# Kernel optimization log

Hardware: AMD Instinct MI355X
Metric: run time of the kernel (lower is better)

Reference implementation:

```python
import jax, jax.numpy as jnp
import numpy as np

NUM_LAYERS = 4
N_EDGE_TYPES = 3
RBAR = 1
DIM = 128
N_NODES = 50000
N_EDGES = 600000
N_HOP_LAYERS = NUM_LAYERS * (NUM_LAYERS + 1) // 2  # 10
EPS = 1e-12


def setup_inputs() -> dict:
    key = jax.random.key(0)
    ks = jax.random.split(key, 8)
    x = jax.random.normal(ks[0], (N_NODES, DIM), dtype=jnp.float32)
    edge_index = jax.random.randint(ks[1], (2, N_EDGES), 0, N_NODES, dtype=jnp.int64)
    edge_hop = jax.random.randint(ks[2], (N_EDGES,), 0, NUM_LAYERS + 1, dtype=jnp.int64)
    edge_type = jax.random.randint(ks[3], (N_EDGES,), 0, N_EDGE_TYPES, dtype=jnp.int64)
    scale = 1.0 / np.sqrt(DIM)
    W_edge = jax.random.normal(ks[4], (N_EDGE_TYPES, DIM, DIM), dtype=jnp.float32) * scale
    b_edge = jnp.zeros((N_EDGE_TYPES, DIM), dtype=jnp.float32)
    W_hop = jax.random.normal(ks[5], (N_HOP_LAYERS, DIM, DIM), dtype=jnp.float32) * scale
    b_hop = jnp.zeros((N_HOP_LAYERS, DIM), dtype=jnp.float32)
    return {"x": x, "edge_index": edge_index, "edge_hop": edge_hop,
            "edge_type": edge_type, "W_edge": W_edge, "b_edge": b_edge,
            "W_hop": W_hop, "b_hop": b_hop}


def _conv(h_in, W, b, src, dst, mask, n_nodes):
    """GraphConv sub-layer on a masked edge subset: sum_{j->i, mask} (x_j W) + b."""
    h = h_in @ W                                  # [N, d]
    msg = h[src] * mask[:, None]                  # [E, d], masked gather
    agg = jax.ops.segment_sum(msg, dst, num_segments=n_nodes)
    return agg + b


def reference(x, edge_index, edge_hop, edge_type, W_edge, b_edge, W_hop, b_hop):
    n_nodes = x.shape[0]
    src, dst = edge_index[0], edge_index[1]
    xs = []
    cur = x
    idx = 0  # sequential consumption of hop sub-layers (next(modules))
    for t in range(NUM_LAYERS):
        xs.append(cur)
        acc = jnp.zeros_like(cur)
        # relation-specific sub-layers, always on x[t]
        for e in range(N_EDGE_TYPES):
            mask = (edge_type == e).astype(cur.dtype)
            acc = acc + _conv(xs[t], W_edge[e], b_edge[e], src, dst, mask, n_nodes)
        # delay / k-hop sub-layers, k = 1..t+1, reading delayed state x[t-delay]
        for k in range(1, t + 2):
            delay = max(k - RBAR, 0)
            mask = (edge_hop == k).astype(cur.dtype)
            acc = acc + _conv(xs[t - delay], W_hop[idx], b_hop[idx], src, dst, mask, n_nodes)
            idx += 1
        cur = xs[t] + jax.nn.relu(acc)
        # F.normalize(p=2, dim=-1): x / max(||x||_2, eps)
        norm = jnp.linalg.norm(cur, axis=-1, keepdims=True)
        cur = cur / jnp.maximum(norm, EPS)
    return cur
```

## Files before the change

kernel.cpp:

```cpp
#include <hip/hip_runtime.h>
#include <hip/hip_bf16.h>

#define DIM 128
#define NLAYER 4

typedef _Float16 f16x8 __attribute__((ext_vector_type(8)));
typedef _Float16 f16x2 __attribute__((ext_vector_type(2)));
typedef float f32x4 __attribute__((ext_vector_type(4)));

static constexpr int PHYS[10] = {0, 4, 1, 0, 5, 2, 1, 4, 6, 3};


__global__ void k_count(const int* __restrict__ dst, int E, int* __restrict__ counts) {
    int e = blockIdx.x * blockDim.x + threadIdx.x;
    if (e < E) atomicAdd(&counts[dst[e]], 1);
}

__global__ __launch_bounds__(1024) void k_scan1(const int* __restrict__ in, int n,
                                                int* __restrict__ partial,
                                                int* __restrict__ blockSums) {
    __shared__ int sd[1024];
    int tid = threadIdx.x;
    int i = blockIdx.x * 1024 + tid;
    int v = (i < n) ? in[i] : 0;
    sd[tid] = v;
    __syncthreads();
    for (int off = 1; off < 1024; off <<= 1) {
        int t = (tid >= off) ? sd[tid - off] : 0;
        __syncthreads();
        sd[tid] += t;
        __syncthreads();
    }
    if (i < n) partial[i] = sd[tid];
    if (tid == 1023) blockSums[blockIdx.x] = sd[1023];
}

__global__ void k_scan2(int* __restrict__ bs, int nb) {
    int lane = threadIdx.x;
    int v = (lane < nb) ? bs[lane] : 0;
    for (int off = 1; off < 64; off <<= 1) {
        int t = __shfl_up(v, off, 64);
        if (lane >= off) v += t;
    }
    int ex = __shfl_up(v, 1, 64);
    if (lane == 0) ex = 0;
    if (lane < nb) bs[lane] = ex;
}

__global__ __launch_bounds__(1024) void k_scan3(const int* __restrict__ partial,
                                                const int* __restrict__ bs, int n,
                                                int* __restrict__ row_ptr,
                                                int* __restrict__ cursor) {
    int i = blockIdx.x * blockDim.x + threadIdx.x;
    if (i < n) {
        int v = partial[i] + bs[i >> 10];
        row_ptr[i + 1] = v;
        cursor[i + 1] = v;
    }
    if (i == 0) { row_ptr[0] = 0; cursor[0] = 0; }
}

__global__ void k_scatter(const int* __restrict__ srcA, const int* __restrict__ dstA,
                          const int* __restrict__ typA, const int* __restrict__ hopA,
                          int E, int* __restrict__ cursor, unsigned* __restrict__ csr) {
    int e = blockIdx.x * blockDim.x + threadIdx.x;
    if (e < E) {
        int d = dstA[e];
        int p = atomicAdd(&cursor[d], 1);
        csr[p] = ((unsigned)srcA[e] << 8) | ((unsigned)typA[e] << 24)
               | ((unsigned)hopA[e] << 26);
    }
}

__global__ void k_bias(const float* __restrict__ b_edge, const float* __restrict__ b_hop,
                       float* __restrict__ bias_sums) {
    int t = blockIdx.x, d = threadIdx.x;
    float s = b_edge[d] + b_edge[DIM + d] + b_edge[2 * DIM + d];
    int base = t * (t + 1) / 2;
    for (int k = 1; k <= t + 1; ++k) s += b_hop[(base + k - 1) * DIM + d];
    bias_sums[t * DIM + d] = s;
}


__global__ void k_convX(const float* __restrict__ in, _Float16* __restrict__ out, int n) {
    int i = (blockIdx.x * blockDim.x + threadIdx.x) * 8;
    if (i >= n) return;
    float4 a = ((const float4*)(in + i))[0];
    float4 b = ((const float4*)(in + i))[1];
    f16x8 o;
    o[0] = (_Float16)a.x; o[1] = (_Float16)a.y; o[2] = (_Float16)a.z; o[3] = (_Float16)a.w;
    o[4] = (_Float16)b.x; o[5] = (_Float16)b.y; o[6] = (_Float16)b.z; o[7] = (_Float16)b.w;
    *(f16x8*)(out + i) = o;
}

__global__ __launch_bounds__(256) void k_convW(const float* __restrict__ W_edge,
                                               const float* __restrict__ W_hop,
                                               _Float16* __restrict__ Wt) {
    int s = blockIdx.x;
    const float* src = (s < 3) ? (W_edge + (size_t)s * DIM * DIM)
                               : (W_hop + (size_t)(s - 3) * DIM * DIM);
    _Float16* dstp = Wt + (size_t)s * DIM * DIM;
    for (int it = 0; it < 64; ++it) {
        int e = it * 256 + threadIdx.x;
        int n = e >> 7, k = e & 127;
        dstp[e] = (_Float16)src[k * DIM + n];
    }
}


struct GatherArgs {
    const _Float16* __restrict__ xt;
    _Float16* __restrict__ Atype;
    _Float16* __restrict__ Ahop;
    const int* __restrict__ row_ptr;
    const unsigned* __restrict__ csr;
    int N;
};

template <int TAU>
__global__ __launch_bounds__(64) void k_gather(GatherArgs a) {
    const int node = blockIdx.x;
    const int lane = threadIdx.x;
    const size_t NS = (size_t)a.N * DIM;

    const char* xtl = (const char*)a.xt + lane * 4;

    float t0x = 0, t0y = 0, t1x = 0, t1y = 0, t2x = 0, t2y = 0;
    float h1x = 0, h1y = 0, h2x = 0, h2y = 0, h3x = 0, h3y = 0, h4x = 0, h4y = 0;

    const int e0 = a.row_ptr[node], e1 = a.row_ptr[node + 1];
    int e = e0;

    #define ACCUM(m, v)                                                        \
        {                                                                      \
            const int typ = (int)((m) >> 24) & 3;                              \
            const int hop = (int)((m) >> 26);                                  \
            const float vx = (float)(v)[0], vy = (float)(v)[1];                \
            if (typ == 0)      { t0x += vx; t0y += vy; }                       \
            else if (typ == 1) { t1x += vx; t1y += vy; }                       \
            else               { t2x += vx; t2y += vy; }                       \
            if (hop == 1)                    { h1x += vx; h1y += vy; }         \
            else if (TAU <= 2 && hop == 2)   { h2x += vx; h2y += vy; }         \
            else if (TAU <= 1 && hop == 3)   { h3x += vx; h3y += vy; }         \
            else if (TAU == 0 && hop == 4)   { h4x += vx; h4y += vy; }         \
        }

    for (; e + 8 <= e1; e += 8) {
        unsigned mm[8];
        #pragma unroll
        for (int j = 0; j < 8; ++j) mm[j] = a.csr[e + j];
        f16x2 vv[8];
        #pragma unroll
        for (int j = 0; j < 8; ++j)
            vv[j] = *(const f16x2*)(xtl + (mm[j] & 0xFFFFFF));
        #pragma unroll
        for (int j = 0; j < 8; ++j) ACCUM(mm[j], vv[j])
    }
    for (; e + 4 <= e1; e += 4) {
        unsigned mm[4];
        #pragma unroll
        for (int j = 0; j < 4; ++j) mm[j] = a.csr[e + j];
        f16x2 vv[4];
        #pragma unroll
        for (int j = 0; j < 4; ++j)
            vv[j] = *(const f16x2*)(xtl + (mm[j] & 0xFFFFFF));
        #pragma unroll
        for (int j = 0; j < 4; ++j) ACCUM(mm[j], vv[j])
    }
    for (; e < e1; ++e) {
        const unsigned m = a.csr[e];
        const f16x2 v = *(const f16x2*)(xtl + (m & 0xFFFFFF));
        ACCUM(m, v)
    }
    #undef ACCUM

    _Float16* tb = a.Atype + (size_t)node * DIM;
    f16x2 o;
    o[0] = (_Float16)t0x; o[1] = (_Float16)t0y; ((f16x2*)(tb + 0 * NS))[lane] = o;
    o[0] = (_Float16)t1x; o[1] = (_Float16)t1y; ((f16x2*)(tb + 1 * NS))[lane] = o;
    o[0] = (_Float16)t2x; o[1] = (_Float16)t2y; ((f16x2*)(tb + 2 * NS))[lane] = o;

    _Float16* hb = a.Ahop + (size_t)node * DIM;
    {
        constexpr int P1 = PHYS[(TAU * (TAU + 1)) / 2];
        o[0] = (_Float16)h1x; o[1] = (_Float16)h1y; ((f16x2*)(hb + (size_t)P1 * NS))[lane] = o;
    }
    if constexpr (TAU <= 2) {
        constexpr int P2 = PHYS[((TAU + 1) * (TAU + 2)) / 2 + 1];
        o[0] = (_Float16)h2x; o[1] = (_Float16)h2y; ((f16x2*)(hb + (size_t)P2 * NS))[lane] = o;
    }
    if constexpr (TAU <= 1) {
        constexpr int P3 = PHYS[((TAU + 2) * (TAU + 3)) / 2 + 2];
        o[0] = (_Float16)h3x; o[1] = (_Float16)h3y; ((f16x2*)(hb + (size_t)P3 * NS))[lane] = o;
    }
    if constexpr (TAU == 0) {
        constexpr int P4 = PHYS[9];
        o[0] = (_Float16)h4x; o[1] = (_Float16)h4y; ((f16x2*)(hb + (size_t)P4 * NS))[lane] = o;
    }
}


struct GemmArgs {
    const _Float16* Aslot[7];
    const _Float16* Wt;
    const _Float16* xin;
    const float* bias;
    float* outf;
    _Float16* outh;
    int N;
    int wsel[7];
};

template <int NSUB>
__global__ __launch_bounds__(128, 2) void k_gemm(GemmArgs a) {
    __shared__ __align__(16) _Float16 Wlds[DIM * DIM];
    const int tid = threadIdx.x, wv = tid >> 6, lane = tid & 63;
    const int rowBase = blockIdx.x * 64 + wv * 32;
    const int lr = lane & 15, lg = lane >> 4;

    int r0 = rowBase + lr, r1 = rowBase + 16 + lr;
    if (r0 >= a.N) r0 = a.N - 1;
    if (r1 >= a.N) r1 = a.N - 1;

    f32x4 acc[2][8];
    #pragma unroll
    for (int rt = 0; rt < 2; ++rt)
        #pragma unroll
        for (int ct = 0; ct < 8; ++ct)
            acc[rt][ct] = (f32x4){0.f, 0.f, 0.f, 0.f};

    const int sw = (lr & 7) << 4;

    {
        const _Float16* Ws = a.Wt + (size_t)a.wsel[0] * (DIM * DIM);
        f16x8 w[16];
        #pragma unroll
        for (int i = 0; i < 16; ++i)
            w[i] = *(const f16x8*)((const char*)Ws + i * 2048 + tid * 16);
        #pragma unroll
        for (int i = 0; i < 16; ++i) {
            const int p = i * 2048 + tid * 16;
            const int q = p ^ (((p >> 8) & 7) << 4);
            *(f16x8*)((char*)Wlds + q) = w[i];
        }
    }
    f16x8 afA[2][4], afB[2][4];
    #pragma unroll
    for (int ks = 0; ks < 4; ++ks) {
        afA[0][ks] = *(const f16x8*)(a.Aslot[0] + (size_t)r0 * DIM + ks * 32 + lg * 8);
        afB[0][ks] = *(const f16x8*)(a.Aslot[0] + (size_t)r1 * DIM + ks * 32 + lg * 8);
    }
    __syncthreads();

    #pragma unroll
    for (int s = 0; s < NSUB; ++s) {
        const int cur = s & 1, nxt = cur ^ 1;
        f16x8 w[16];
        if (s + 1 < NSUB) {
            const _Float16* Wn = a.Wt + (size_t)a.wsel[s + 1] * (DIM * DIM);
            #pragma unroll
            for (int i = 0; i < 16; ++i)
                w[i] = *(const f16x8*)((const char*)Wn + i * 2048 + tid * 16);
            const _Float16* An = a.Aslot[s + 1];
            #pragma unroll
            for (int ks = 0; ks < 4; ++ks) {
                afA[nxt][ks] = *(const f16x8*)(An + (size_t)r0 * DIM + ks * 32 + lg * 8);
                afB[nxt][ks] = *(const f16x8*)(An + (size_t)r1 * DIM + ks * 32 + lg * 8);
            }
        }
        #pragma unroll
        for (int ks = 0; ks < 4; ++ks) {
            const int cb = (ks * 32 + lg * 8) * 2;
            #pragma unroll
            for (int ct = 0; ct < 8; ++ct) {
                const int addr = (ct * 16 + lr) * 256 + (cb ^ sw);
                const f16x8 bf = *(const f16x8*)((const char*)Wlds + addr);
                acc[0][ct] = __builtin_amdgcn_mfma_f32_16x16x32_f16(afA[cur][ks], bf, acc[0][ct], 0, 0, 0);
                acc[1][ct] = __builtin_amdgcn_mfma_f32_16x16x32_f16(afB[cur][ks], bf, acc[1][ct], 0, 0, 0);
            }
        }
        __syncthreads();
        if (s + 1 < NSUB) {
            #pragma unroll
            for (int i = 0; i < 16; ++i) {
                const int p = i * 2048 + tid * 16;
                const int q = p ^ (((p >> 8) & 7) << 4);
                *(f16x8*)((char*)Wlds + q) = w[i];
            }
            __syncthreads();
        }
    }

    float bv[8];
    #pragma unroll
    for (int ct = 0; ct < 8; ++ct) bv[ct] = a.bias[ct * 16 + lr];

    #pragma unroll
    for (int rt = 0; rt < 2; ++rt) {
        #pragma unroll
        for (int rg = 0; rg < 4; ++rg) {
            const int row = rowBase + rt * 16 + lg * 4 + rg;
            const int rr = (row < a.N) ? row : a.N - 1;
            float v[8];
            float ss = 0.f;
            #pragma unroll
            for (int ct = 0; ct < 8; ++ct) {
                const float xval = (float)a.xin[(size_t)rr * DIM + ct * 16 + lr];
                const float tv = fmaxf(acc[rt][ct][rg] + bv[ct], 0.f) + xval;
                v[ct] = tv;
                ss += tv * tv;
            }
            ss += __shfl_xor(ss, 1, 64);
            ss += __shfl_xor(ss, 2, 64);
            ss += __shfl_xor(ss, 4, 64);
            ss += __shfl_xor(ss, 8, 64);
            const float inv = 1.f / fmaxf(sqrtf(ss), 1e-12f);
            if (row < a.N) {
                #pragma unroll
                for (int ct = 0; ct < 8; ++ct) {
                    const int col = ct * 16 + lr;
                    const float ov = v[ct] * inv;
                    if (a.outf) a.outf[(size_t)row * DIM + col] = ov;
                    if (a.outh) a.outh[(size_t)row * DIM + col] = (_Float16)ov;
                }
            }
        }
    }
}


static inline size_t align_up(size_t v, size_t a) { return (v + a - 1) & ~(a - 1); }

extern "C" void kernel_launch(void* const* d_in, const int* in_sizes, int n_in,
                              void* d_out, int out_size, void* d_ws, size_t ws_size,
                              hipStream_t stream) {
    const float* x        = (const float*)d_in[0];
    const int* edge_index = (const int*)d_in[1];
    const int* edge_hop   = (const int*)d_in[2];
    const int* edge_type  = (const int*)d_in[3];
    const float* W_edge   = (const float*)d_in[4];
    const float* b_edge   = (const float*)d_in[5];
    const float* W_hop    = (const float*)d_in[6];
    const float* b_hop    = (const float*)d_in[7];
    float* out = (float*)d_out;

    int N = in_sizes[0] / DIM;
    int E = in_sizes[2];
    const int* srcA = edge_index;
    const int* dstA = edge_index + E;

    size_t NSh = (size_t)N * DIM * sizeof(_Float16);
    size_t off = 0;
    char* wsb = (char*)d_ws;
    _Float16* xh0     = (_Float16*)(wsb + off);  off = align_up(off + NSh, 64);
    _Float16* xh1     = (_Float16*)(wsb + off);  off = align_up(off + NSh, 64);
    _Float16* xh2     = (_Float16*)(wsb + off);  off = align_up(off + NSh, 64);
    _Float16* xh3     = (_Float16*)(wsb + off);  off = align_up(off + NSh, 64);
    _Float16* Atype   = (_Float16*)(wsb + off);  off = align_up(off + 3 * NSh, 64);
    _Float16* Ahop    = (_Float16*)(wsb + off);  off = align_up(off + 7 * NSh, 64);
    _Float16* Wt      = (_Float16*)(wsb + off);  off = align_up(off + 13 * DIM * DIM * sizeof(_Float16), 64);
    int* counts       = (int*)(wsb + off);       off = align_up(off + (size_t)N * 4, 64);
    int* partial      = (int*)(wsb + off);       off = align_up(off + (size_t)N * 4, 64);
    int* blockSums    = (int*)(wsb + off);       off = align_up(off + 64 * 4, 64);
    int* row_ptr      = (int*)(wsb + off);       off = align_up(off + (size_t)(N + 1) * 4, 64);
    int* cursor       = (int*)(wsb + off);       off = align_up(off + (size_t)(N + 1) * 4, 64);
    unsigned* csr     = (unsigned*)(wsb + off);  off = align_up(off + (size_t)E * 4, 64);
    float* bias_sums  = (float*)(wsb + off);     off = align_up(off + 4 * DIM * 4, 64);
    (void)ws_size;

    hipMemsetAsync(counts, 0, (size_t)N * 4, stream);
    k_count<<<(E + 255) / 256, 256, 0, stream>>>(dstA, E, counts);
    int nb = (N + 1023) / 1024;
    k_scan1<<<nb, 1024, 0, stream>>>(counts, N, partial, blockSums);
    k_scan2<<<1, 64, 0, stream>>>(blockSums, nb);
    k_scan3<<<nb, 1024, 0, stream>>>(partial, blockSums, N, row_ptr, cursor);
    k_scatter<<<(E + 255) / 256, 256, 0, stream>>>(srcA, dstA, edge_type, edge_hop, E, cursor, csr);
    k_bias<<<4, DIM, 0, stream>>>(b_edge, b_hop, bias_sums);

    k_convX<<<(N * DIM / 8 + 255) / 256, 256, 0, stream>>>(x, xh0, N * DIM);
    k_convW<<<13, 256, 0, stream>>>(W_edge, W_hop, Wt);

    _Float16* xh_ptr[4] = { xh0, xh1, xh2, xh3 };
    const size_t NS = (size_t)N * DIM;

    for (int t = 0; t < NLAYER; ++t) {
        GatherArgs g;
        g.xt = xh_ptr[t];
        g.Atype = Atype; g.Ahop = Ahop;
        g.row_ptr = row_ptr; g.csr = csr; g.N = N;
        switch (t) {
            case 0: k_gather<0><<<N, 64, 0, stream>>>(g); break;
            case 1: k_gather<1><<<N, 64, 0, stream>>>(g); break;
            case 2: k_gather<2><<<N, 64, 0, stream>>>(g); break;
            default: k_gather<3><<<N, 64, 0, stream>>>(g); break;
        }

        GemmArgs m;
        m.Wt = Wt; m.xin = xh_ptr[t];
        m.bias = bias_sums + t * DIM;
        m.outf = (t == 3) ? out : nullptr;
        m.outh = (t < 3) ? xh_ptr[t + 1] : nullptr;
        m.N = N;
        const int nsub = t + 4;
        const int base = t * (t + 1) / 2;
        for (int s = 0; s < 3; ++s) { m.wsel[s] = s; m.Aslot[s] = Atype + (size_t)s * NS; }
        for (int j = 0; j <= t; ++j) {
            m.wsel[3 + j] = 3 + base + j;
            m.Aslot[3 + j] = Ahop + (size_t)PHYS[base + j] * NS;
        }
        for (int s = nsub; s < 7; ++s) { m.wsel[s] = 0; m.Aslot[s] = Atype; }

        const int gb = (N + 63) / 64;
        switch (nsub) {
            case 4: k_gemm<4><<<gb, 128, 0, stream>>>(m); break;
            case 5: k_gemm<5><<<gb, 128, 0, stream>>>(m); break;
            case 6: k_gemm<6><<<gb, 128, 0, stream>>>(m); break;
            default: k_gemm<7><<<gb, 128, 0, stream>>>(m); break;
        }
    }
}
```

Baseline: 343.6 us.

## Build the CSR with a two-level bucket sort using shared-memory atomics

Replaces the per-edge global-atomic count and scatter CSR build with a two-pass bucket sort. The first pass makes per-chunk histograms over 256-node buckets. The second scatters packed (dst, payload) words into bucket order using LDS cursors. A per-bucket finalize kernel then counts, scans and reorders the edges locally in shared memory, writing row_ptr and csr. The aim is to avoid contended global atomics and the random global writes of the old scatter. In exchange it adds an 8-byte intermediate buffer and one extra pass, and relies on each bucket fitting in the 8192-entry staging array.

Result: faster. 298.7 us (-13.1%).

```diff
diff --git a/kernel.cpp b/kernel.cpp
--- a/kernel.cpp
+++ b/kernel.cpp
@@ -3,6 +3,7 @@
 
 #define DIM 128
 #define NLAYER 4
+#define CHUNK 4096
 
 typedef _Float16 f16x8 __attribute__((ext_vector_type(8)));
 typedef _Float16 f16x2 __attribute__((ext_vector_type(2)));
@@ -11,9 +12,19 @@
 static constexpr int PHYS[10] = {0, 4, 1, 0, 5, 2, 1, 4, 6, 3};
 
 
-__global__ void k_count(const int* __restrict__ dst, int E, int* __restrict__ counts) {
-    int e = blockIdx.x * blockDim.x + threadIdx.x;
-    if (e < E) atomicAdd(&counts[dst[e]], 1);
+__global__ __launch_bounds__(256) void k_hist1(const int* __restrict__ dst, int E,
+                                               int B1, int NBKT, int* __restrict__ ghist) {
+    __shared__ int h[256];
+    h[threadIdx.x] = 0;
+    __syncthreads();
+    const int base = blockIdx.x * CHUNK;
+    #pragma unroll
+    for (int i = 0; i < CHUNK / 256; ++i) {
+        int e = base + i * 256 + threadIdx.x;
+        if (e < E) atomicAdd(&h[dst[e] >> 8], 1);
+    }
+    __syncthreads();
+    if (threadIdx.x < NBKT) ghist[threadIdx.x * B1 + blockIdx.x] = h[threadIdx.x];
 }
 
 __global__ __launch_bounds__(1024) void k_scan1(const int* __restrict__ in, int n,
@@ -47,29 +58,78 @@
     if (lane < nb) bs[lane] = ex;
 }
 
-__global__ __launch_bounds__(1024) void k_scan3(const int* __restrict__ partial,
-                                                const int* __restrict__ bs, int n,
-                                                int* __restrict__ row_ptr,
-                                                int* __restrict__ cursor) {
+__global__ __launch_bounds__(1024) void k_scan3b(const int* __restrict__ partial,
+                                                 const int* __restrict__ bs, int n,
+                                                 int* __restrict__ outEx) {
     int i = blockIdx.x * blockDim.x + threadIdx.x;
-    if (i < n) {
-        int v = partial[i] + bs[i >> 10];
-        row_ptr[i + 1] = v;
-        cursor[i + 1] = v;
-    }
-    if (i == 0) { row_ptr[0] = 0; cursor[0] = 0; }
-}
-
-__global__ void k_scatter(const int* __restrict__ srcA, const int* __restrict__ dstA,
-                          const int* __restrict__ typA, const int* __restrict__ hopA,
-                          int E, int* __restrict__ cursor, unsigned* __restrict__ csr) {
-    int e = blockIdx.x * blockDim.x + threadIdx.x;
-    if (e < E) {
-        int d = dstA[e];
-        int p = atomicAdd(&cursor[d], 1);
-        csr[p] = ((unsigned)srcA[e] << 8) | ((unsigned)typA[e] << 24)
-               | ((unsigned)hopA[e] << 26);
-    }
+    if (i < n) outEx[i + 1] = partial[i] + bs[i >> 10];
+    if (i == 0) outEx[0] = 0;
+}
+
+__global__ __launch_bounds__(256) void k_scat1(const int* __restrict__ srcA,
+                                               const int* __restrict__ dstA,
+                                               const int* __restrict__ typA,
+                                               const int* __restrict__ hopA,
+                                               int E, int B1, int NBKT,
+                                               const int* __restrict__ gcur,
+                                               unsigned long long* __restrict__ ebuf) {
+    __shared__ int cur[256];
+    if (threadIdx.x < NBKT) cur[threadIdx.x] = gcur[threadIdx.x * B1 + blockIdx.x];
+    __syncthreads();
+    const int base = blockIdx.x * CHUNK;
+    #pragma unroll
+    for (int i = 0; i < CHUNK / 256; ++i) {
+        int e = base + i * 256 + threadIdx.x;
+        if (e < E) {
+            int d = dstA[e];
+            unsigned w = ((unsigned)srcA[e] << 8) | ((unsigned)typA[e] << 24)
+                       | ((unsigned)hopA[e] << 26);
+            int p = atomicAdd(&cur[d >> 8], 1);
+            ebuf[p] = ((unsigned long long)(unsigned)d << 32) | w;
+        }
+    }
+}
+
+__global__ __launch_bounds__(256) void k_finalize(const unsigned long long* __restrict__ ebuf,
+                                                  const int* __restrict__ gcur,
+                                                  int E, int B1, int NBKT, int N,
+                                                  unsigned* __restrict__ csr,
+                                                  int* __restrict__ row_ptr) {
+    __shared__ int cnt[256], sd[256], off2[256];
+    __shared__ unsigned stg[8192];
+    const int bkt = blockIdx.x, tid = threadIdx.x;
+    const int base = gcur[bkt * B1];
+    const int endv = (bkt + 1 < NBKT) ? gcur[(bkt + 1) * B1] : E;
+    const int n = endv - base;
+
+    cnt[tid] = 0;
+    __syncthreads();
+    for (int i = tid; i < n; i += 256)
+        atomicAdd(&cnt[(int)((ebuf[base + i] >> 32) & 255)], 1);
+    __syncthreads();
+
+    sd[tid] = cnt[tid];
+    __syncthreads();
+    for (int o = 1; o < 256; o <<= 1) {
+        int t = (tid >= o) ? sd[tid - o] : 0;
+        __syncthreads();
+        sd[tid] += t;
+        __syncthreads();
+    }
+    const int ex = (tid > 0) ? sd[tid - 1] : 0;
+    off2[tid] = ex;
+    const int node = bkt * 256 + tid;
+    if (node < N) row_ptr[node] = base + ex;
+    if (bkt == NBKT - 1 && tid == 0) row_ptr[N] = E;
+    __syncthreads();
+
+    for (int i = tid; i < n; i += 256) {
+        const unsigned long long ld = ebuf[base + i];
+        const int r = atomicAdd(&off2[(int)((ld >> 32) & 255)], 1);
+        stg[r] = (unsigned)ld;
+    }
+    __syncthreads();
+    for (int i = tid; i < n; i += 256) csr[base + i] = stg[i];
 }
 
 __global__ void k_bias(const float* __restrict__ b_edge, const float* __restrict__ b_hop,
@@ -349,6 +409,10 @@
     const int* srcA = edge_index;
     const int* dstA = edge_index + E;
 
+    const int B1 = (E + CHUNK - 1) / CHUNK;
+    const int NBKT = (N + 255) >> 8;
+    const int n2 = NBKT * B1;
+
     size_t NSh = (size_t)N * DIM * sizeof(_Float16);
     size_t off = 0;
     char* wsb = (char*)d_ws;
@@ -359,22 +423,24 @@
     _Float16* Atype   = (_Float16*)(wsb + off);  off = align_up(off + 3 * NSh, 64);
     _Float16* Ahop    = (_Float16*)(wsb + off);  off = align_up(off + 7 * NSh, 64);
     _Float16* Wt      = (_Float16*)(wsb + off);  off = align_up(off + 13 * DIM * DIM * sizeof(_Float16), 64);
-    int* counts       = (int*)(wsb + off);       off = align_up(off + (size_t)N * 4, 64);
-    int* partial      = (int*)(wsb + off);       off = align_up(off + (size_t)N * 4, 64);
+    int* ghist        = (int*)(wsb + off);       off = align_up(off + (size_t)n2 * 4, 64);
+    int* partial      = (int*)(wsb + off);       off = align_up(off + (size_t)n2 * 4, 64);
     int* blockSums    = (int*)(wsb + off);       off = align_up(off + 64 * 4, 64);
+    int* gcur         = (int*)(wsb + off);       off = align_up(off + (size_t)(n2 + 1) * 4, 64);
     int* row_ptr      = (int*)(wsb + off);       off = align_up(off + (size_t)(N + 1) * 4, 64);
-    int* cursor       = (int*)(wsb + off);       off = align_up(off + (size_t)(N + 1) * 4, 64);
+    unsigned long long* ebuf = (unsigned long long*)(wsb + off);
+                                                 off = align_up(off + (size_t)E * 8, 64);
     unsigned* csr     = (unsigned*)(wsb + off);  off = align_up(off + (size_t)E * 4, 64);
     float* bias_sums  = (float*)(wsb + off);     off = align_up(off + 4 * DIM * 4, 64);
     (void)ws_size;
 
-    hipMemsetAsync(counts, 0, (size_t)N * 4, stream);
-    k_count<<<(E + 255) / 256, 256, 0, stream>>>(dstA, E, counts);
-    int nb = (N + 1023) / 1024;
-    k_scan1<<<nb, 1024, 0, stream>>>(counts, N, partial, blockSums);
-    k_scan2<<<1, 64, 0, stream>>>(blockSums, nb);
-    k_scan3<<<nb, 1024, 0, stream>>>(partial, blockSums, N, row_ptr, cursor);
-    k_scatter<<<(E + 255) / 256, 256, 0, stream>>>(srcA, dstA, edge_type, edge_hop, E, cursor, csr);
+    k_hist1<<<B1, 256, 0, stream>>>(dstA, E, B1, NBKT, ghist);
+    int nb2 = (n2 + 1023) / 1024;
+    k_scan1<<<nb2, 1024, 0, stream>>>(ghist, n2, partial, blockSums);
+    k_scan2<<<1, 64, 0, stream>>>(blockSums, nb2);
+    k_scan3b<<<nb2, 1024, 0, stream>>>(partial, blockSums, n2, gcur);
+    k_scat1<<<B1, 256, 0, stream>>>(srcA, dstA, edge_type, edge_hop, E, B1, NBKT, gcur, ebuf);
+    k_finalize<<<NBKT, 256, 0, stream>>>(ebuf, gcur, E, B1, NBKT, N, csr, row_ptr);
     k_bias<<<4, DIM, 0, stream>>>(b_edge, b_hop, bias_sums);
 
     k_convX<<<(N * DIM / 8 + 255) / 256, 256, 0, stream>>>(x, xh0, N * DIM);
```
